# Optimization experiments

Hardware: AMD Instinct MI355X
Metric: run time of the kernel (lower is better)

Reference implementation:

```python
import jax, jax.numpy as jnp
import numpy as np

# irreps config: (multiplicity, l) for "128x0e + 64x1o + 32x2e" (in == out)
IRREPS = [(128, 0), (64, 1), (32, 2)]


def setup_inputs() -> dict:
    key = jax.random.key(0)
    k0, k1, k2, k3 = jax.random.split(key, 4)
    N = 200000
    dim = sum(mul * (2 * l + 1) for mul, l in IRREPS)  # 480
    x = jax.random.normal(k0, (N, dim), dtype=jnp.float32)
    W0 = jax.random.normal(k1, (128, 128), dtype=jnp.float32)
    W1 = jax.random.normal(k2, (64, 64), dtype=jnp.float32)
    W2 = jax.random.normal(k3, (32, 32), dtype=jnp.float32)
    return {"x": x, "W0": W0, "W1": W1, "W2": W2}


def _irrep_linear(x, weights):
    # x: [N, dim_in]; per-irrep: reshape block to [N, mul, 2l+1], contract mul dim,
    # scale by 1/sqrt(fan_in) = 1/sqrt(mul_in) (e3nn default path normalization).
    outs = []
    off = 0
    for (mul, l), W in zip(IRREPS, weights):
        d = 2 * l + 1
        blk = x[:, off:off + mul * d].reshape(-1, mul, d)  # [N, mul, d]
        alpha = 1.0 / np.sqrt(mul)
        y = jnp.einsum('nid,io->nod', blk, W) * jnp.float32(alpha)  # [N, mul_out, d]
        outs.append(y.reshape(-1, mul * d))
        off += mul * d
    return jnp.concatenate(outs, axis=-1)  # [N, dim_out]


def reference(x, W0, W1, W2):
    return _irrep_linear(x, (W0, W1, W2))
```

## Files before the change

### kernel.cpp

```cpp
#include <hip/hip_runtime.h>

typedef _Float16 v8h __attribute__((ext_vector_type(8)));
typedef float    v4f __attribute__((ext_vector_type(4)));

#define MFMA16(a, b, c) __builtin_amdgcn_mfma_f32_16x16x32_f16((a), (b), (c), 0, 0, 0)

#define GLL16(gptr, lptr)                                                        \
  __builtin_amdgcn_global_load_lds((const __attribute__((address_space(1))) void*)(gptr), \
                                   (__attribute__((address_space(3))) void*)(lptr), 16, 0, 0)


__global__ void build_frags_k(const float* __restrict__ W0, const float* __restrict__ W1,
                              const float* __restrict__ W2, v8h* __restrict__ frag) {
  const int f = blockIdx.x;
  const int lane = threadIdx.x;
  int ot, kt;
  if (f < 32)       { ot = f >> 2;           kt = f & 3; }
  else if (f < 104) { int q = f - 32;  ot = 8 + q / 6;  kt = 4 + q % 6; }
  else              { int q = f - 104; ot = 20 + q / 5; kt = 10 + q % 5; }
  const int n  = ot * 16 + (lane & 15);
  const int kb = kt * 32 + (lane >> 4) * 8;
  v8h v;
#pragma unroll
  for (int e = 0; e < 8; ++e) {
    const int k = kb + e;
    float wv = 0.0f;
    if (k < 128) {
      if (n < 128) wv = W0[k * 128 + n] * 0.08838834764831845f;
    } else if (k < 320) {
      if (n >= 128 && n < 320) {
        const int i = k - 128, o = n - 128;
        if (i % 3 == o % 3) wv = W1[(i / 3) * 64 + (o / 3)] * 0.125f;
      }
    } else {
      if (n >= 320) {
        const int i = k - 320, o = n - 320;
        if (i % 5 == o % 5) wv = W2[(i / 5) * 32 + (o / 5)] * 0.17677669529663687f;
      }
    }
    v[e] = (_Float16)wv;
  }
  frag[f * 64 + lane] = v;
}

template <int V, int G>
__device__ __forceinline__ void wave_main(const float* __restrict__ x,
                                          const v8h* __restrict__ frag,
                                          float* __restrict__ out,
                                          unsigned char* sm, int t, int b, int nc) {
  const int lane = t & 63;
  const int w    = t >> 6;
  const int r16  = lane & 15;
  const int g    = lane >> 4;

  constexpr int S  = (V == 0) ? 8 : (V == 1) ? 6 : 10;
  constexpr int NF = (V == 0) ? 16 : (V == 1) ? 18 : 25;

  v8h f[NF];
  if constexpr (V == 0) {
#pragma unroll
    for (int i = 0; i < 4; ++i)
#pragma unroll
      for (int k = 0; k < 4; ++k)
        f[i * 4 + k] = frag[((w + 2 * i) * 4 + k) * 64 + lane];
  } else if constexpr (V == 1) {
#pragma unroll
    for (int i = 0; i < 3; ++i)
#pragma unroll
      for (int k = 0; k < 6; ++k)
        f[i * 6 + k] = frag[(32 + (w - 2 + 4 * i) * 6 + k) * 64 + lane];
  } else {
#pragma unroll
    for (int i = 0; i < 5; ++i)
#pragma unroll
      for (int k = 0; k < 5; ++k)
        f[i * 5 + k] = frag[(104 + (w - 6 + 2 * i) * 5 + k) * 64 + lane];
  }

  auto stage = [&](int tt, int bsel) {
    const unsigned char* xt = (const unsigned char*)x + (size_t)tt * 61440u;
    unsigned char* buf = sm + bsel * 61440;
#pragma unroll
    for (int i = 0; i < 8; ++i) {
      if (i < 7 || t < 256) {
        const unsigned gl = (unsigned)(i * 512 + t);
        const unsigned r  = gl / 120u;
        const unsigned j  = gl - r * 120u;
        GLL16(xt + r * 1920u + ((j ^ (r & 7u)) << 4), buf + i * 8192 + w * 1024);
      }
    }
  };

#define LDAF(kt, dst)                                                                       \
  {                                                                                         \
    const unsigned j0 = (unsigned)((kt) * 8 + g * 2);                                       \
    const float4 lo = *reinterpret_cast<const float4*>(smc + rb + (((j0) ^ q) << 4));       \
    const float4 hi = *reinterpret_cast<const float4*>(smc + rb + ((((j0) + 1) ^ q) << 4)); \
    v8h v_;                                                                                 \
    v_[0] = (_Float16)lo.x; v_[1] = (_Float16)lo.y;                                         \
    v_[2] = (_Float16)lo.z; v_[3] = (_Float16)lo.w;                                         \
    v_[4] = (_Float16)hi.x; v_[5] = (_Float16)hi.y;                                         \
    v_[6] = (_Float16)hi.z; v_[7] = (_Float16)hi.w;                                         \
    dst = v_;                                                                               \
  }

  auto compute = [&](int tt, int bsel) {
    const unsigned char* smc = sm + bsel * 61440;
#pragma unroll
    for (int sl = 0; sl < 2; ++sl) {
      const unsigned row = (unsigned)(sl * 16 + r16);
      const unsigned rb  = row * 1920u;
      const unsigned q   = row & 7u;
      float* const ob = out + ((size_t)tt * 32 + sl * 16 + r16) * 480 + g * 4;
      if constexpr (V == 0) {
        v8h xr[4];
#pragma unroll
        for (int k = 0; k < 4; ++k) LDAF(k, xr[k]);
#pragma unroll
        for (int i = 0; i < 4; ++i) {
          v4f a = {0.f, 0.f, 0.f, 0.f};
#pragma unroll
          for (int k = 0; k < 4; ++k) a = MFMA16(f[i * 4 + k], xr[k], a);
          *reinterpret_cast<v4f*>(ob + (w + 2 * i) * 16) = a;
        }
      } else if constexpr (V == 1) {
        v8h xr[6];
#pragma unroll
        for (int k = 0; k < 6; ++k) LDAF(4 + k, xr[k]);
#pragma unroll
        for (int i = 0; i < 3; ++i) {
          v4f a = {0.f, 0.f, 0.f, 0.f};
#pragma unroll
          for (int k = 0; k < 6; ++k) a = MFMA16(f[i * 6 + k], xr[k], a);
          *reinterpret_cast<v4f*>(ob + (6 + w + 4 * i) * 16) = a;
        }
      } else {
        v8h xr[5];
#pragma unroll
        for (int k = 0; k < 5; ++k) LDAF(10 + k, xr[k]);
#pragma unroll
        for (int i = 0; i < 5; ++i) {
          v4f a = {0.f, 0.f, 0.f, 0.f};
#pragma unroll
          for (int k = 0; k < 5; ++k) a = MFMA16(f[i * 5 + k], xr[k], a);
          *reinterpret_cast<v4f*>(ob + (14 + w + 2 * i) * 16) = a;
        }
      }
    }
  };

  stage(b, 0);
  stage(b + 256, 1);
  asm volatile("s_waitcnt vmcnt(%0)" :: "n"(G) : "memory");
  __builtin_amdgcn_s_barrier();
  compute(b, 0);
  __builtin_amdgcn_s_barrier();

  int c = 1;
  for (; c < nc - 1; ++c) {
    stage(b + (c + 1) * 256, (c + 1) & 1);
    asm volatile("s_waitcnt vmcnt(%0)" :: "n"(G + S) : "memory");
    __builtin_amdgcn_s_barrier();
    compute(b + c * 256, c & 1);
    __builtin_amdgcn_s_barrier();
  }
  {
    asm volatile("s_waitcnt vmcnt(%0)" :: "n"(S) : "memory");
    __builtin_amdgcn_s_barrier();
    compute(b + c * 256, c & 1);
  }
#undef LDAF
}

__global__ __launch_bounds__(512, 1) void irrep_linear_k(
    const float* __restrict__ x, const v8h* __restrict__ frag, float* __restrict__ out,
    int n_tiles) {
  __shared__ __align__(16) unsigned char sm[2 * 61440];
  const int t = threadIdx.x;
  const int b = blockIdx.x;
  const int nc = (n_tiles - b + 255) >> 8;
  const int w = t >> 6;
  if (w < 2)      wave_main<0, 8>(x, frag, out, sm, t, b, nc);
  else if (w < 4) wave_main<1, 8>(x, frag, out, sm, t, b, nc);
  else if (w < 6) wave_main<1, 7>(x, frag, out, sm, t, b, nc);
  else            wave_main<2, 7>(x, frag, out, sm, t, b, nc);
}

extern "C" void kernel_launch(void* const* d_in, const int* in_sizes, int n_in,
                              void* d_out, int out_size, void* d_ws, size_t ws_size,
                              hipStream_t stream) {
  const float* x  = (const float*)d_in[0];
  const float* W0 = (const float*)d_in[1];
  const float* W1 = (const float*)d_in[2];
  const float* W2 = (const float*)d_in[3];
  float* out = (float*)d_out;
  v8h* frag = (v8h*)d_ws;

  build_frags_k<<<154, 64, 0, stream>>>(W0, W1, W2, frag);

  const int N = in_sizes[0] / 480;
  const int n_tiles = N / 32;
  irrep_linear_k<<<256, 512, 0, stream>>>(x, frag, out, n_tiles);
}
```

Measured before the change: 155.7 us.

## Halve tile rows and deepen LDS pipeline to four stages

Tiles shrink from 32 to 16 rows (30 KB each), and the LDS ring grows from two slots to four. Loads now run two tiles ahead of compute, and the trailing barrier after each compute step is removed, since a slot is only reused two iterations later. The aim is to keep more global loads in flight and hide latency better in this bandwidth-bound kernel, at the cost of more barriers per byte and smaller compute steps. The vmcnt arithmetic has been re-derived, and an error there would cause races.

After: 150.0 us, median of 2. 1.04x faster.

```diff
diff --git a/kernel.cpp b/kernel.cpp
--- a/kernel.cpp
+++ b/kernel.cpp
@@ -53,7 +53,7 @@
   const int r16  = lane & 15;
   const int g    = lane >> 4;
 
-  constexpr int S  = (V == 0) ? 8 : (V == 1) ? 6 : 10;
+  constexpr int S  = (V == 0) ? 4 : (V == 1) ? 3 : 5;
   constexpr int NF = (V == 0) ? 16 : (V == 1) ? 18 : 25;
 
   v8h f[NF];
@@ -77,12 +77,12 @@
         f[i * 5 + k] = frag[(104 + (w - 6 + 2 * i) * 5 + k) * 64 + lane];
   }
 
-  auto stage = [&](int tt, int bsel) {
-    const unsigned char* xt = (const unsigned char*)x + (size_t)tt * 61440u;
-    unsigned char* buf = sm + bsel * 61440;
+  auto stage = [&](int tt, int slot) {
+    const unsigned char* xt = (const unsigned char*)x + (size_t)tt * 30720u;
+    unsigned char* buf = sm + (size_t)slot * 30720u;
 #pragma unroll
-    for (int i = 0; i < 8; ++i) {
-      if (i < 7 || t < 256) {
+    for (int i = 0; i < 4; ++i) {
+      if (i < 3 || w < 6) {
         const unsigned gl = (unsigned)(i * 512 + t);
         const unsigned r  = gl / 120u;
         const unsigned j  = gl - r * 120u;
@@ -104,86 +104,79 @@
     dst = v_;                                                                               \
   }
 
-  auto compute = [&](int tt, int bsel) {
-    const unsigned char* smc = sm + bsel * 61440;
+  auto compute = [&](int tt, int slot) {
+    const unsigned char* smc = sm + (size_t)slot * 30720u;
+    const unsigned rb = (unsigned)r16 * 1920u;
+    const unsigned q  = (unsigned)(r16 & 7u);
+    float* const ob = out + ((size_t)tt * 16 + r16) * 480 + g * 4;
+    if constexpr (V == 0) {
+      v8h xr[4];
 #pragma unroll
-    for (int sl = 0; sl < 2; ++sl) {
-      const unsigned row = (unsigned)(sl * 16 + r16);
-      const unsigned rb  = row * 1920u;
-      const unsigned q   = row & 7u;
-      float* const ob = out + ((size_t)tt * 32 + sl * 16 + r16) * 480 + g * 4;
-      if constexpr (V == 0) {
-        v8h xr[4];
+      for (int k = 0; k < 4; ++k) LDAF(k, xr[k]);
 #pragma unroll
-        for (int k = 0; k < 4; ++k) LDAF(k, xr[k]);
+      for (int i = 0; i < 4; ++i) {
+        v4f a = {0.f, 0.f, 0.f, 0.f};
 #pragma unroll
-        for (int i = 0; i < 4; ++i) {
-          v4f a = {0.f, 0.f, 0.f, 0.f};
+        for (int k = 0; k < 4; ++k) a = MFMA16(f[i * 4 + k], xr[k], a);
+        *reinterpret_cast<v4f*>(ob + (w + 2 * i) * 16) = a;
+      }
+    } else if constexpr (V == 1) {
+      v8h xr[6];
 #pragma unroll
-          for (int k = 0; k < 4; ++k) a = MFMA16(f[i * 4 + k], xr[k], a);
-          *reinterpret_cast<v4f*>(ob + (w + 2 * i) * 16) = a;
-        }
-      } else if constexpr (V == 1) {
-        v8h xr[6];
+      for (int k = 0; k < 6; ++k) LDAF(4 + k, xr[k]);
 #pragma unroll
-        for (int k = 0; k < 6; ++k) LDAF(4 + k, xr[k]);
+      for (int i = 0; i < 3; ++i) {
+        v4f a = {0.f, 0.f, 0.f, 0.f};
 #pragma unroll
-        for (int i = 0; i < 3; ++i) {
-          v4f a = {0.f, 0.f, 0.f, 0.f};
+        for (int k = 0; k < 6; ++k) a = MFMA16(f[i * 6 + k], xr[k], a);
+        *reinterpret_cast<v4f*>(ob + (6 + w + 4 * i) * 16) = a;
+      }
+    } else {
+      v8h xr[5];
 #pragma unroll
-          for (int k = 0; k < 6; ++k) a = MFMA16(f[i * 6 + k], xr[k], a);
-          *reinterpret_cast<v4f*>(ob + (6 + w + 4 * i) * 16) = a;
-        }
-      } else {
-        v8h xr[5];
+      for (int k = 0; k < 5; ++k) LDAF(10 + k, xr[k]);
 #pragma unroll
-        for (int k = 0; k < 5; ++k) LDAF(10 + k, xr[k]);
+      for (int i = 0; i < 5; ++i) {
+        v4f a = {0.f, 0.f, 0.f, 0.f};
 #pragma unroll
-        for (int i = 0; i < 5; ++i) {
-          v4f a = {0.f, 0.f, 0.f, 0.f};
-#pragma unroll
-          for (int k = 0; k < 5; ++k) a = MFMA16(f[i * 5 + k], xr[k], a);
-          *reinterpret_cast<v4f*>(ob + (14 + w + 2 * i) * 16) = a;
-        }
+        for (int k = 0; k < 5; ++k) a = MFMA16(f[i * 5 + k], xr[k], a);
+        *reinterpret_cast<v4f*>(ob + (14 + w + 2 * i) * 16) = a;
       }
     }
   };
 
+#define PIPE(C, N)                                              \
+  {                                                             \
+    asm volatile("s_waitcnt vmcnt(%0)" :: "n"(N) : "memory");   \
+    __builtin_amdgcn_s_barrier();                               \
+    compute(b + (C) * 256, (C) & 3);                            \
+  }
+
   stage(b, 0);
   stage(b + 256, 1);
-  asm volatile("s_waitcnt vmcnt(%0)" :: "n"(G) : "memory");
-  __builtin_amdgcn_s_barrier();
-  compute(b, 0);
-  __builtin_amdgcn_s_barrier();
-
-  int c = 1;
-  for (; c < nc - 1; ++c) {
-    stage(b + (c + 1) * 256, (c + 1) & 1);
-    asm volatile("s_waitcnt vmcnt(%0)" :: "n"(G + S) : "memory");
-    __builtin_amdgcn_s_barrier();
-    compute(b + c * 256, c & 1);
-    __builtin_amdgcn_s_barrier();
+  stage(b + 2 * 256, 2); PIPE(0, 2 * G)
+  stage(b + 3 * 256, 3); PIPE(1, 2 * G + S)
+  for (int c = 2; c <= nc - 3; ++c) {
+    stage(b + (c + 2) * 256, (c + 2) & 3);
+    PIPE(c, 2 * G + 2 * S)
   }
-  {
-    asm volatile("s_waitcnt vmcnt(%0)" :: "n"(S) : "memory");
-    __builtin_amdgcn_s_barrier();
-    compute(b + c * 256, c & 1);
-  }
+  PIPE(nc - 2, G + 2 * S)
+  PIPE(nc - 1, 2 * S)
+#undef PIPE
 #undef LDAF
 }
 
 __global__ __launch_bounds__(512, 1) void irrep_linear_k(
     const float* __restrict__ x, const v8h* __restrict__ frag, float* __restrict__ out,
     int n_tiles) {
-  __shared__ __align__(16) unsigned char sm[2 * 61440];
+  __shared__ __align__(16) unsigned char sm[4 * 30720];
   const int t = threadIdx.x;
   const int b = blockIdx.x;
   const int nc = (n_tiles - b + 255) >> 8;
   const int w = t >> 6;
-  if (w < 2)      wave_main<0, 8>(x, frag, out, sm, t, b, nc);
-  else if (w < 4) wave_main<1, 8>(x, frag, out, sm, t, b, nc);
-  else if (w < 6) wave_main<1, 7>(x, frag, out, sm, t, b, nc);
-  else            wave_main<2, 7>(x, frag, out, sm, t, b, nc);
+  if (w < 2)      wave_main<0, 4>(x, frag, out, sm, t, b, nc);
+  else if (w < 6) wave_main<1, 4>(x, frag, out, sm, t, b, nc);
+  else            wave_main<2, 3>(x, frag, out, sm, t, b, nc);
 }
 
 extern "C" void kernel_launch(void* const* d_in, const int* in_sizes, int n_in,
@@ -199,6 +192,6 @@
   build_frags_k<<<154, 64, 0, stream>>>(W0, W1, W2, frag);
 
   const int N = in_sizes[0] / 480;
-  const int n_tiles = N / 32;
+  const int n_tiles = N / 16;
   irrep_linear_k<<<256, 512, 0, stream>>>(x, frag, out, n_tiles);
 }
```
